# Performance work log

Hardware: AMD Instinct MI355X
Metric: run time of the kernel (lower is better)

The kernel has to match this reference:

```python
import jax, jax.numpy as jnp
import numpy as np

DIM = 1024
DIM_FEAT = 384
HIDDEN = 1024
HEADS = 16
D_HEAD = HIDDEN // HEADS
SCALE = D_HEAD ** -0.5
EPS = 1e-5


def _layernorm(x, g, b):
    mu = jnp.mean(x, axis=-1, keepdims=True)
    var = jnp.var(x, axis=-1, keepdims=True)
    return (x - mu) * jax.lax.rsqrt(var + EPS) * g + b


def _split_heads(t):
    b, n, _ = t.shape
    return t.reshape(b, n, HEADS, D_HEAD).transpose(0, 2, 1, 3)  # b h n d


def _merge_heads(t):
    b, h, n, d = t.shape
    return t.transpose(0, 2, 1, 3).reshape(b, n, h * d)


def _attn(q, k, v):
    dots = jnp.einsum('bhnd,bhmd->bhnm', q, k) * SCALE
    attn = jax.nn.softmax(dots, axis=-1)
    return jnp.einsum('bhnm,bhmd->bhnd', attn, v)


def setup_inputs() -> dict:
    key = jax.random.key(0)
    ks = jax.random.split(key, 10)
    B, N = 2, 2048
    s = lambda fan: 1.0 / np.sqrt(fan)
    return {
        'x': jax.random.normal(ks[0], (B, N, DIM), jnp.float32),
        'feature': jax.random.normal(ks[1], (B, N, DIM_FEAT), jnp.float32),
        'norm_g': jnp.ones((DIM,), jnp.float32),
        'norm_b': jnp.zeros((DIM,), jnp.float32),
        'W_cq': jax.random.normal(ks[2], (DIM, HIDDEN), jnp.float32) * s(DIM),
        'W_ckv': jax.random.normal(ks[3], (DIM_FEAT, 2 * HIDDEN), jnp.float32) * s(DIM_FEAT),
        'W_sqkv': jax.random.normal(ks[4], (DIM, 3 * HIDDEN), jnp.float32) * s(DIM),
        'ffn_g': jnp.ones((DIM,), jnp.float32),
        'ffn_b': jnp.zeros((DIM,), jnp.float32),
        'W1': jax.random.normal(ks[5], (DIM, 4 * DIM), jnp.float32) * s(DIM),
        'b1': jnp.zeros((4 * DIM,), jnp.float32),
        'W2': jax.random.normal(ks[6], (4 * DIM, DIM), jnp.float32) * s(4 * DIM),
        'b2': jnp.zeros((DIM,), jnp.float32),
    }


def reference(x, feature, norm_g, norm_b, W_cq, W_ckv, W_sqkv, ffn_g, ffn_b, W1, b1, W2, b2):
    # cross attention
    xn = _layernorm(x, norm_g, norm_b)
    q = _split_heads(xn @ W_cq)
    kv = feature @ W_ckv
    k, v = jnp.split(kv, 2, axis=-1)
    cross = _merge_heads(_attn(q, _split_heads(k), _split_heads(v))) + x
    # self attention (shared norm)
    cn = _layernorm(cross, norm_g, norm_b)
    qkv = cn @ W_sqkv
    sq, sk, sv = (_split_heads(t) for t in jnp.split(qkv, 3, axis=-1))
    self_tok = _merge_heads(_attn(sq, sk, sv)) + cross
    # FFN with its own layernorm
    h = _layernorm(self_tok, ffn_g, ffn_b)
    h = jax.nn.gelu(h @ W1 + b1, approximate=False)
    out = h @ W2 + b2
    return out + self_tok
```

## Files before the change

kernel.cpp:

```cpp
#include <hip/hip_runtime.h>
#include <math.h>
#include <stdint.h>

typedef __attribute__((ext_vector_type(8)))  short   short8;
typedef __attribute__((ext_vector_type(4)))  short   short4v;
typedef __attribute__((ext_vector_type(8)))  __bf16  bf16x8;
typedef __attribute__((ext_vector_type(4)))  float   f32x4;
typedef __attribute__((ext_vector_type(16))) float   f32x16;

__device__ __forceinline__ unsigned short f2b(float f) {
    union { float f; unsigned u; } v; v.f = f;
    unsigned r = v.u + 0x7FFF + ((v.u >> 16) & 1);
    return (unsigned short)(r >> 16);
}

__device__ __forceinline__ float b2f(unsigned short u) {
    union { unsigned u; float f; } v; v.u = (unsigned)u << 16; return v.f;
}

__device__ __forceinline__ f32x4 mfma_bf16(bf16x8 a, bf16x8 b, f32x4 c) {
    return __builtin_amdgcn_mfma_f32_16x16x32_bf16(a, b, c, 0, 0, 0);
}

__device__ __forceinline__ f32x16 mfma32(bf16x8 a, bf16x8 b, f32x16 c) {
    return __builtin_amdgcn_mfma_f32_32x32x16_bf16(a, b, c, 0, 0, 0);
}

__device__ __forceinline__ unsigned cvt_pk_bf16(float lo, float hi) {
    unsigned r;
    asm volatile("v_cvt_pk_bf16_f32 %0, %1, %2" : "=v"(r) : "v"(lo), "v"(hi));
    return r;
}

__device__ __forceinline__ void gload_lds16(const unsigned short* g, unsigned short* l) {
    __builtin_amdgcn_global_load_lds(
        (const __attribute__((address_space(1))) void*)g,
        (__attribute__((address_space(3))) void*)l,
        16, 0, 0);
}

template <int N>
__device__ __forceinline__ void wait_vmcnt() {
    if constexpr (N == 0)       asm volatile("s_waitcnt vmcnt(0)" ::: "memory");
    else if constexpr (N == 4)  asm volatile("s_waitcnt vmcnt(4)" ::: "memory");
    else if constexpr (N == 6)  asm volatile("s_waitcnt vmcnt(6)" ::: "memory");
    else if constexpr (N == 8)  asm volatile("s_waitcnt vmcnt(8)" ::: "memory");
    else                        static_assert(N == 0 || N == 4 || N == 6 || N == 8, "add vmcnt case");
}

#define QSCALE 0.18033688011112042592f

__global__ __launch_bounds__(256) void wconv_t(const float* __restrict__ W,
                                               unsigned short* __restrict__ Wt,
                                               int K, int N) {
    __shared__ float tile[32][33];
    int bk = blockIdx.x * 32;
    int bn = blockIdx.y * 32;
    int tx = threadIdx.x & 31, ty = threadIdx.x >> 5;
#pragma unroll
    for (int i = 0; i < 4; ++i) {
        int r = ty + i * 8;
        tile[r][tx] = W[(size_t)(bk + r) * N + bn + tx];
    }
    __syncthreads();
#pragma unroll
    for (int i = 0; i < 4; ++i) {
        int r = ty + i * 8;
        Wt[(size_t)(bn + r) * K + bk + tx] = f2b(tile[tx][r]);
    }
}

__global__ __launch_bounds__(256) void fconv(const float* __restrict__ in,
                                             unsigned short* __restrict__ out, int n4) {
    int i = blockIdx.x * 256 + threadIdx.x;
    if (i >= n4) return;
    f32x4 v = ((const f32x4*)in)[i];
    short4v o;
    o.x = (short)f2b(v.x); o.y = (short)f2b(v.y);
    o.z = (short)f2b(v.z); o.w = (short)f2b(v.w);
    ((short4v*)out)[i] = o;
}

__global__ __launch_bounds__(256) void lnorm(const float* __restrict__ x,
                                             const float* __restrict__ g,
                                             const float* __restrict__ bta,
                                             unsigned short* __restrict__ out) {
    int row = blockIdx.x;
    const f32x4* xr = (const f32x4*)(x + (size_t)row * 1024);
    int t = threadIdx.x;
    f32x4 v = xr[t];
    float s  = v.x + v.y + v.z + v.w;
    float s2 = v.x * v.x + v.y * v.y + v.z * v.z + v.w * v.w;
#pragma unroll
    for (int m = 1; m < 64; m <<= 1) {
        s  += __shfl_xor(s, m);
        s2 += __shfl_xor(s2, m);
    }
    __shared__ float rs[8];
    int w = t >> 6;
    if ((t & 63) == 0) { rs[w] = s; rs[4 + w] = s2; }
    __syncthreads();
    s  = rs[0] + rs[1] + rs[2] + rs[3];
    s2 = rs[4] + rs[5] + rs[6] + rs[7];
    float mean = s * (1.0f / 1024.0f);
    float var  = s2 * (1.0f / 1024.0f) - mean * mean;
    float rstd = rsqrtf(var + 1e-5f);
    f32x4 gv = ((const f32x4*)g)[t];
    f32x4 bv = ((const f32x4*)bta)[t];
    short4v o;
    o.x = (short)f2b((v.x - mean) * rstd * gv.x + bv.x);
    o.y = (short)f2b((v.y - mean) * rstd * gv.y + bv.y);
    o.z = (short)f2b((v.z - mean) * rstd * gv.z + bv.z);
    o.w = (short)f2b((v.w - mean) * rstd * gv.w + bv.w);
    ((short4v*)(out + (size_t)row * 1024))[t] = o;
}

template <int WM, int WN, int MI, int NI, int EPI, bool SCQ>
__global__ __launch_bounds__(WM * WN * 64, 2)
void gemm8(const unsigned short* __restrict__ A,
           const unsigned short* __restrict__ Bt,
           void* __restrict__ C,
           const float* __restrict__ bias,
           const float* __restrict__ resid,
           int M, int N, int K, int scale_cols) {
    constexpr int BM = WM * MI * 16;
    constexpr int BN = WN * NI * 16;
    constexpr int THREADS = WM * WN * 64;
    constexpr int ROWS = THREADS / 8;
    constexpr int IA = BM / ROWS;
    constexpr int IB = BN / ROWS;

    const int nwg = gridDim.x;
    const int nby = N / BN;
    int flat = blockIdx.x;
    int wk = (flat & 7) * (nwg >> 3) + (flat >> 3);
    const int m0 = (wk / nby) * BM;
    const int n0 = (wk % nby) * BN;

    __shared__ unsigned short As[2][BM * 64];
    __shared__ unsigned short Bs[2][BN * 64];

    const int tid  = threadIdx.x;
    const int lane = tid & 63;
    const int wid  = tid >> 6;
    const int wm = wid / WN, wn = wid % WN;
    const int l15 = lane & 15, q4 = lane >> 4, xw = lane & 7;

    const int sr = tid >> 3;
    const int sg = (tid & 7) ^ (sr & 7);

    const unsigned short* ag = A  + (size_t)(m0 + sr) * K + sg * 8;
    const unsigned short* bg = Bt + (size_t)(n0 + sr) * K + sg * 8;

    f32x4 acc[MI][NI] = {};

    auto STAGE = [&](int d, int t) {
        const int k0 = t * 64;
#pragma unroll
        for (int i = 0; i < IA; ++i)
            gload_lds16(ag + (size_t)(i * ROWS) * K + k0, &As[d][i * ROWS * 64 + tid * 8]);
#pragma unroll
        for (int i = 0; i < IB; ++i)
            gload_lds16(bg + (size_t)(i * ROWS) * K + k0, &Bs[d][i * ROWS * 64 + tid * 8]);
    };

    const int NT = K >> 6;
    STAGE(0, 0);

    for (int t = 0; t < NT; ++t) {
        const int c = t & 1;
        if (t + 1 < NT) STAGE(c ^ 1, t + 1);
        __builtin_amdgcn_sched_barrier(0);
        if (t + 1 < NT) wait_vmcnt<IA + IB>();
        else            wait_vmcnt<0>();
        __builtin_amdgcn_s_barrier();
        __builtin_amdgcn_sched_barrier(0);
#pragma unroll
        for (int h = 0; h < 2; ++h) {
            bf16x8 a[MI], b[NI];
            const int gsl = h * 4 + q4;
#pragma unroll
            for (int mi = 0; mi < MI; ++mi)
                a[mi] = *(const bf16x8*)&As[c][(wm * MI * 16 + mi * 16 + l15) * 64 + ((gsl ^ xw) << 3)];
#pragma unroll
            for (int ni = 0; ni < NI; ++ni)
                b[ni] = *(const bf16x8*)&Bs[c][(wn * NI * 16 + ni * 16 + l15) * 64 + ((gsl ^ xw) << 3)];
            __builtin_amdgcn_s_setprio(1);
#pragma unroll
            for (int mi = 0; mi < MI; ++mi)
#pragma unroll
                for (int ni = 0; ni < NI; ++ni)
                    acc[mi][ni] = mfma_bf16(a[mi], b[ni], acc[mi][ni]);
            __builtin_amdgcn_s_setprio(0);
        }
        __builtin_amdgcn_sched_barrier(0);
        __builtin_amdgcn_s_barrier();
    }

    const int rb = m0 + wm * MI * 16 + q4 * 4;
    const int cb = n0 + wn * NI * 16 + l15;
    float bv[NI];
    if (EPI >= 1) {
#pragma unroll
        for (int ni = 0; ni < NI; ++ni) bv[ni] = bias[cb + ni * 16];
    }
#pragma unroll
    for (int mi = 0; mi < MI; ++mi) {
#pragma unroll
        for (int r = 0; r < 4; ++r) {
            const int row = rb + mi * 16 + r;
#pragma unroll
            for (int ni = 0; ni < NI; ++ni) {
                const int col = cb + ni * 16;
                float v = acc[mi][ni][r];
                if (EPI == 0) {
                    if (SCQ && col < scale_cols) v *= QSCALE;
                    ((unsigned short*)C)[(size_t)row * N + col] = f2b(v);
                } else if (EPI == 1) {
                    v += bv[ni];
                    v = 0.5f * v * (1.0f + erff(v * 0.70710678118f));
                    ((unsigned short*)C)[(size_t)row * N + col] = f2b(v);
                } else {
                    v += bv[ni] + resid[(size_t)row * N + col];
                    ((float*)C)[(size_t)row * N + col] = v;
                }
            }
        }
    }
}

template <int EPI, bool SCQ, int KSPLIT>
__global__ __launch_bounds__(512, 2)
void gemm256(const unsigned short* __restrict__ A,
             const unsigned short* __restrict__ Bt,
             void* __restrict__ C,
             const float* __restrict__ bias,
             unsigned short* __restrict__ ph0,
             unsigned short* __restrict__ ph1,
             int M, int N, int lda, int ldb, int klen, int scale_cols) {
    const int nby = N / 256;
    const int nmn = (M / 256) * nby;
    const int nwg = gridDim.x;
    int flat = blockIdx.x;
    int wk = (flat & 7) * (nwg >> 3) + (flat >> 3);
    int ks = 0;
    if constexpr (KSPLIT > 1) { ks = wk / nmn; wk -= ks * nmn; }
    const int m0 = (wk / nby) * 256;
    const int n0 = (wk % nby) * 256;
    const int koff = ks * klen;

    __shared__ unsigned short As[2][256 * 64];
    __shared__ unsigned short Bs[2][256 * 64];

    const int tid  = threadIdx.x;
    const int lane = tid & 63;
    const int wid  = tid >> 6;
    const int wm = wid >> 2, wn = wid & 3;
    const int l15 = lane & 15, q4 = lane >> 4, xw = lane & 7;

    const int sr = tid >> 3;
    const int sg = (tid & 7) ^ (sr & 7);

    const unsigned short* ag = A  + (size_t)(m0 + sr) * lda + koff + sg * 8;
    const unsigned short* bg = Bt + (size_t)(n0 + sr) * ldb + koff + sg * 8;

    f32x4 acc[8][4] = {};

#define SA256(d, t, i) gload_lds16(ag + (size_t)((i) * 64) * lda + (t) * 64, &As[d][(i) * 4096 + tid * 8])
#define SB256(d, t, i) gload_lds16(bg + (size_t)((i) * 64) * ldb + (t) * 64, &Bs[d][(i) * 4096 + tid * 8])

    const int NT = klen >> 6;
#pragma unroll
    for (int i = 0; i < 4; ++i) { SA256(0, 0, i); SB256(0, 0, i); }
    __syncthreads();

    for (int t = 0; t < NT; ++t) {
        const int c = t & 1;
        if (t + 1 < NT) {
#pragma unroll
            for (int i = 0; i < 4; ++i) { SA256(c ^ 1, t + 1, i); SB256(c ^ 1, t + 1, i); }
        }
        bf16x8 breg[4];
#pragma unroll
        for (int p = 0; p < 4; ++p) {
            const int h = p >> 1, mh = p & 1;
            const int col = ((h * 4 + q4) ^ xw) << 3;
            if ((p & 1) == 0) {
#pragma unroll
                for (int ni = 0; ni < 4; ++ni)
                    breg[ni] = *(const bf16x8*)&Bs[c][(wn * 64 + ni * 16 + l15) * 64 + col];
            }
            bf16x8 a[4];
#pragma unroll
            for (int mi = 0; mi < 4; ++mi)
                a[mi] = *(const bf16x8*)&As[c][(wm * 128 + mh * 64 + mi * 16 + l15) * 64 + col];
#pragma unroll
            for (int mi = 0; mi < 4; ++mi)
#pragma unroll
                for (int ni = 0; ni < 4; ++ni)
                    acc[mh * 4 + mi][ni] = mfma_bf16(a[mi], breg[ni], acc[mh * 4 + mi][ni]);
        }
        __syncthreads();
    }
#undef SA256
#undef SB256

    const int rb = m0 + wm * 128 + q4 * 4;
    const int cb = n0 + wn * 64 + l15;
    float bv[4];
    if (EPI == 1) {
#pragma unroll
        for (int ni = 0; ni < 4; ++ni) bv[ni] = bias[cb + ni * 16];
    }
    unsigned short* pb = nullptr;
    if (EPI == 3) pb = ((ks & 2) ? ph1 : ph0) + (size_t)(ks & 1) * ((size_t)M * N);
#pragma unroll
    for (int ai = 0; ai < 8; ++ai) {
#pragma unroll
        for (int r = 0; r < 4; ++r) {
            const int row = rb + ai * 16 + r;
#pragma unroll
            for (int ni = 0; ni < 4; ++ni) {
                const int col = cb + ni * 16;
                float v = acc[ai][ni][r];
                if (EPI == 0) {
                    if (SCQ && col < scale_cols) v *= QSCALE;
                    ((unsigned short*)C)[(size_t)row * N + col] = f2b(v);
                } else if (EPI == 1) {
                    v += bv[ni];
                    v = 0.5f * v * (1.0f + erff(v * 0.70710678118f));
                    ((unsigned short*)C)[(size_t)row * N + col] = f2b(v);
                } else {
                    pb[(size_t)row * N + col] = f2b(v);
                }
            }
        }
    }
}

__global__ __launch_bounds__(256) void kmerge(const unsigned short* __restrict__ p01,
                                              const unsigned short* __restrict__ p23,
                                              const float* __restrict__ bias,
                                              float* __restrict__ out) {
    const size_t i4 = (size_t)blockIdx.x * 256 + threadIdx.x;
    const size_t e = i4 * 4;
    const int col4 = (int)(e & 1023);
    f32x4 acc = *(const f32x4*)&bias[col4];
    const size_t MN = (size_t)4096 * 1024;
#pragma unroll
    for (int k = 0; k < 2; ++k) {
        short4v a = *(const short4v*)&p01[k * MN + e];
        short4v b = *(const short4v*)&p23[k * MN + e];
        acc.x += b2f((unsigned short)a.x) + b2f((unsigned short)b.x);
        acc.y += b2f((unsigned short)a.y) + b2f((unsigned short)b.y);
        acc.z += b2f((unsigned short)a.z) + b2f((unsigned short)b.z);
        acc.w += b2f((unsigned short)a.w) + b2f((unsigned short)b.w);
    }
    f32x4 o = *(const f32x4*)&out[e];
    o.x += acc.x; o.y += acc.y; o.z += acc.z; o.w += acc.w;
    *(f32x4*)&out[e] = o;
}

__global__ __launch_bounds__(256) void kvpack(const unsigned short* __restrict__ src,
                                              int stride, int k_off, int v_off,
                                              unsigned short* __restrict__ pack) {
    const int oct = blockIdx.x;
    const int bh  = blockIdx.y;
    const int b = bh >> 4, h = bh & 15;
    const int tid = threadIdx.x;
    const int lane = tid & 63;
    const int sl = tid >> 6;
    const int l31 = lane & 31, l5 = lane >> 5;
    __shared__ unsigned short Kl[32 * 64], Vl[32 * 64];
    const int r = tid >> 3, c8 = (tid & 7) * 8;
    for (int t8 = 0; t8 < 8; ++t8) {
        const int kt = oct * 8 + t8;
        const int kb = kt * 32;
        *(short8*)&Kl[r * 64 + c8] = *(const short8*)&src[(size_t)(b * 2048 + kb + r) * stride + k_off + h * 64 + c8];
        *(short8*)&Vl[r * 64 + c8] = *(const short8*)&src[(size_t)(b * 2048 + kb + r) * stride + v_off + h * 64 + c8];
        __syncthreads();
        unsigned short* o = pack + (size_t)bh * 262144 + (size_t)kt * 4096;
        *(short8*)&o[sl * 512 + lane * 8] = *(const short8*)&Kl[l31 * 64 + sl * 16 + l5 * 8];
        {
            const int dh = sl >> 1, c2 = sl & 1;
            short8 vv;
#pragma unroll
            for (int j = 0; j < 8; ++j)
                vv[j] = (short)Vl[(c2 * 16 + l5 * 8 + j) * 64 + dh * 32 + l31];
            *(short8*)&o[(4 + sl) * 512 + lane * 8] = vv;
        }
        __syncthreads();
    }
}

__global__ __launch_bounds__(256) void attn(const unsigned short* __restrict__ Q, int q_stride, int q_off,
                                            const unsigned short* __restrict__ pack,
                                            const float* __restrict__ res,
                                            float* __restrict__ out) {
    const int bid = blockIdx.x;
    const int slot = bid >> 3;
    const int bh = (bid & 7) * 4 + (slot >> 5);
    const int qt = slot & 31;
    const int b = bh >> 4, h = bh & 15;
    const int tid = threadIdx.x;
    const int lane = tid & 63, w = tid >> 6;
    const int qg = w >> 1, ks = w & 1;
    const int l31 = lane & 31, l5 = lane >> 5;

    __shared__ unsigned short lds[2][8192];

    const int q0 = qt * 64 + qg * 32;

    const unsigned short* qp = Q + (size_t)(b * 2048 + q0 + l31) * q_stride + q_off + h * 64 + l5 * 8;
    bf16x8 qf[4];
#pragma unroll
    for (int i = 0; i < 4; ++i) qf[i] = *(const bf16x8*)&qp[i * 16];

    const unsigned short* pkb = pack + (size_t)bh * 262144;

    f32x16 oacc[2] = {};
    f32x16 lacc = {};

    auto STAGE = [&](int d, int t) {
        const unsigned short* s = pkb + (size_t)t * 8192;
#pragma unroll
        for (int i = 0; i < 4; ++i) {
            const int ch = i * 4 + w;
            gload_lds16(s + ch * 512 + lane * 8, &lds[d][ch * 512 + lane * 8]);
        }
    };

    STAGE(0, 0);

    for (int t = 0; t < 32; ++t) {
        const int cur = t & 1;
        if (t + 1 < 32) STAGE(cur ^ 1, t + 1);
        __builtin_amdgcn_sched_barrier(0);
        if (t + 1 < 32) wait_vmcnt<4>();
        else            wait_vmcnt<0>();
        __builtin_amdgcn_s_barrier();
        __builtin_amdgcn_sched_barrier(0);

        const unsigned short* L = &lds[cur][ks * 4096 + lane * 8];

        bf16x8 kf[4];
#pragma unroll
        for (int i = 0; i < 4; ++i) kf[i] = *(const bf16x8*)&L[i * 512];

        f32x16 s = {};
        __builtin_amdgcn_s_setprio(1);
#pragma unroll
        for (int i = 0; i < 4; ++i) s = mfma32(kf[i], qf[i], s);
        __builtin_amdgcn_s_setprio(0);

        bf16x8 vf[2][2];
#pragma unroll
        for (int dh = 0; dh < 2; ++dh)
#pragma unroll
            for (int c2 = 0; c2 < 2; ++c2)
                vf[dh][c2] = *(const bf16x8*)&L[(4 + dh * 2 + c2) * 512];

        float p[16];
#pragma unroll
        for (int r = 0; r < 16; ++r) p[r] = __builtin_amdgcn_exp2f(s[r]);
#pragma unroll
        for (int r = 0; r < 16; ++r) lacc[r] += p[r];

        bf16x8 pf[2];
#pragma unroll
        for (int c = 0; c < 2; ++c) {
            unsigned a0 = cvt_pk_bf16(p[8 * c + 0], p[8 * c + 1]);
            unsigned a1 = cvt_pk_bf16(p[8 * c + 4], p[8 * c + 5]);
            unsigned b0 = cvt_pk_bf16(p[8 * c + 2], p[8 * c + 3]);
            unsigned b1 = cvt_pk_bf16(p[8 * c + 6], p[8 * c + 7]);
            asm volatile("v_permlane32_swap_b32 %0, %1" : "+v"(a0), "+v"(a1));
            asm volatile("v_permlane32_swap_b32 %0, %1" : "+v"(b0), "+v"(b1));
            union { unsigned u[4]; bf16x8 v; } pu;
            pu.u[0] = a0; pu.u[1] = b0; pu.u[2] = a1; pu.u[3] = b1;
            pf[c] = pu.v;
        }

        __builtin_amdgcn_s_setprio(1);
#pragma unroll
        for (int dh = 0; dh < 2; ++dh)
#pragma unroll
            for (int c2 = 0; c2 < 2; ++c2)
                oacc[dh] = mfma32(vf[dh][c2], pf[c2], oacc[dh]);
        __builtin_amdgcn_s_setprio(0);

        __builtin_amdgcn_s_barrier();
    }

    float lsum[16];
#pragma unroll
    for (int r = 0; r < 16; ++r) lsum[r] = lacc[r];
#pragma unroll
    for (int off = 8; off >= 1; off >>= 1)
#pragma unroll
        for (int r = 0; r < off; ++r) lsum[r] += lsum[r + off];
    float lh = lsum[0] + __shfl_xor(lsum[0], 32);

    float* mb = (float*)&lds[qg][0];
    if (ks == 1) {
#pragma unroll
        for (int dh = 0; dh < 2; ++dh)
#pragma unroll
            for (int r = 0; r < 16; ++r)
                mb[lane * 33 + dh * 16 + r] = oacc[dh][r];
        mb[lane * 33 + 32] = lh;
    }
    __syncthreads();
    if (ks == 0) {
#pragma unroll
        for (int dh = 0; dh < 2; ++dh)
#pragma unroll
            for (int r = 0; r < 16; ++r)
                oacc[dh][r] += mb[lane * 33 + dh * 16 + r];
        const float l = lh + mb[lane * 33 + 32];

        const float inv = 1.0f / l;
        const size_t rowoff = (size_t)(b * 2048 + q0 + l31) * 1024 + h * 64;
#pragma unroll
        for (int dh = 0; dh < 2; ++dh) {
#pragma unroll
            for (int g = 0; g < 4; ++g) {
                const int col = dh * 32 + g * 8 + l5 * 4;
                f32x4 rv = *(const f32x4*)&res[rowoff + col];
                f32x4 ov;
#pragma unroll
                for (int r = 0; r < 4; ++r) ov[r] = oacc[dh][g * 4 + r] * inv + rv[r];
                *(f32x4*)&out[rowoff + col] = ov;
            }
        }
    }
}

extern "C" void kernel_launch(void* const* d_in, const int* in_sizes, int n_in,
                              void* d_out, int out_size, void* d_ws, size_t ws_size,
                              hipStream_t stream) {
    const float* x      = (const float*)d_in[0];
    const float* feat   = (const float*)d_in[1];
    const float* norm_g = (const float*)d_in[2];
    const float* norm_b = (const float*)d_in[3];
    const float* W_cq   = (const float*)d_in[4];
    const float* W_ckv  = (const float*)d_in[5];
    const float* W_sqkv = (const float*)d_in[6];
    const float* ffn_g  = (const float*)d_in[7];
    const float* ffn_b  = (const float*)d_in[8];
    const float* W1     = (const float*)d_in[9];
    const float* b1     = (const float*)d_in[10];
    const float* W2     = (const float*)d_in[11];
    const float* b2     = (const float*)d_in[12];
    float* out = (float*)d_out;

    char* ws = (char*)d_ws;
    unsigned short* wq_t   = (unsigned short*)(ws + (size_t)(0u)   * (1u << 20));
    unsigned short* wkv_t  = (unsigned short*)(ws + (size_t)(2u)   * (1u << 20));
    unsigned short* wqkv_t = (unsigned short*)(ws + (size_t)(4u)   * (1u << 20));
    unsigned short* w1_t   = (unsigned short*)(ws + (size_t)(10u)  * (1u << 20));
    unsigned short* w2_t   = (unsigned short*)(ws + (size_t)(18u)  * (1u << 20));
    unsigned short* featb  = (unsigned short*)(ws + (size_t)(26u)  * (1u << 20));
    unsigned short* t0     = (unsigned short*)(ws + (size_t)(29u)  * (1u << 20));
    float*          cross  = (float*)        (ws + (size_t)(37u)  * (1u << 20));
    unsigned short* qb     = (unsigned short*)(ws + (size_t)(53u)  * (1u << 20));
    unsigned short* kvb    = (unsigned short*)(ws + (size_t)(61u)  * (1u << 20));
    unsigned short* qkvb   = (unsigned short*)(ws + (size_t)(77u)  * (1u << 20));
    unsigned short* packb  = (unsigned short*)(ws + (size_t)(101u) * (1u << 20));
    unsigned short* h1     = (unsigned short*)(ws + (size_t)(53u)  * (1u << 20));
    unsigned short* part01 = (unsigned short*)(ws + (size_t)(37u)  * (1u << 20));
    unsigned short* part23 = (unsigned short*)(ws + (size_t)(101u) * (1u << 20));

    wconv_t<<<dim3(1024 / 32, 1024 / 32), 256, 0, stream>>>(W_cq,   wq_t,   1024, 1024);
    wconv_t<<<dim3(384 / 32,  2048 / 32), 256, 0, stream>>>(W_ckv,  wkv_t,  384,  2048);
    wconv_t<<<dim3(1024 / 32, 3072 / 32), 256, 0, stream>>>(W_sqkv, wqkv_t, 1024, 3072);
    wconv_t<<<dim3(1024 / 32, 4096 / 32), 256, 0, stream>>>(W1,     w1_t,   1024, 4096);
    wconv_t<<<dim3(4096 / 32, 1024 / 32), 256, 0, stream>>>(W2,     w2_t,   4096, 1024);
    fconv<<<dim3((4096 * 384 / 4) / 256), 256, 0, stream>>>(feat, featb, 4096 * 384 / 4);

    lnorm<<<4096, 256, 0, stream>>>(x, norm_g, norm_b, t0);
    gemm8<2, 2, 4, 2, 0, true ><<<512, 256, 0, stream>>>(t0,    wq_t,  qb,  nullptr, nullptr, 4096, 1024, 1024, 1024);
    gemm8<2, 2, 4, 4, 0, false><<<512, 256, 0, stream>>>(featb, wkv_t, kvb, nullptr, nullptr, 4096, 2048, 384,  0);
    kvpack<<<dim3(8, 32), 256, 0, stream>>>(kvb, 2048, 0, 1024, packb);
    attn<<<1024, 256, 0, stream>>>(qb, 1024, 0, packb, x, cross);

    lnorm<<<4096, 256, 0, stream>>>(cross, norm_g, norm_b, t0);
    gemm256<0, true , 1><<<192, 512, 0, stream>>>(t0, wqkv_t, qkvb, nullptr, nullptr, nullptr, 4096, 3072, 1024, 1024, 1024, 1024);
    kvpack<<<dim3(8, 32), 256, 0, stream>>>(qkvb, 3072, 1024, 2048, packb);
    attn<<<1024, 256, 0, stream>>>(qkvb, 3072, 0, packb, cross, out);

    lnorm<<<4096, 256, 0, stream>>>(out, ffn_g, ffn_b, t0);
    gemm256<1, false, 1><<<256, 512, 0, stream>>>(t0, w1_t, h1, b1, nullptr, nullptr, 4096, 4096, 1024, 1024, 1024, 0);
    gemm256<3, false, 4><<<256, 512, 0, stream>>>(h1, w2_t, nullptr, nullptr, part01, part23, 4096, 1024, 4096, 4096, 1024, 0);
    kmerge<<<4096, 256, 0, stream>>>(part01, part23, b2, out);
}
```

Baseline: 329.7 us.

## Split 256x256 GEMM tiles into half-buffers with phased prefetch and vmcnt waits

Restructures the 256x256 bf16 GEMM main loop into four phases. Each phase loads one 128-row half of A or B for the next k-step, waits with a fine-grained vmcnt instead of a full __syncthreads, and raises wave priority around its MFMA block. The warp-to-output mapping also changes, so each wave now owns four 16-row blocks in each M half and two 16-column blocks in each N half. The aim is to overlap global-to-LDS loads with MFMA work and cut barrier stalls, at the cost of more barriers per k-step and a more fragile wait-count scheme.

New measurement: 322.6 us, median of 4. -2.2%, faster.

```diff
diff --git a/kernel.cpp b/kernel.cpp
--- a/kernel.cpp
+++ b/kernel.cpp
@@ -42,10 +42,11 @@
 template <int N>
 __device__ __forceinline__ void wait_vmcnt() {
     if constexpr (N == 0)       asm volatile("s_waitcnt vmcnt(0)" ::: "memory");
+    else if constexpr (N == 2)  asm volatile("s_waitcnt vmcnt(2)" ::: "memory");
     else if constexpr (N == 4)  asm volatile("s_waitcnt vmcnt(4)" ::: "memory");
     else if constexpr (N == 6)  asm volatile("s_waitcnt vmcnt(6)" ::: "memory");
     else if constexpr (N == 8)  asm volatile("s_waitcnt vmcnt(8)" ::: "memory");
-    else                        static_assert(N == 0 || N == 4 || N == 6 || N == 8, "add vmcnt case");
+    else                        static_assert(N <= 8, "add vmcnt case");
 }
 
 #define QSCALE 0.18033688011112042592f
@@ -249,8 +250,8 @@
     const int n0 = (wk % nby) * 256;
     const int koff = ks * klen;
 
-    __shared__ unsigned short As[2][256 * 64];
-    __shared__ unsigned short Bs[2][256 * 64];
+    __shared__ unsigned short Ah[2][2][128 * 64];
+    __shared__ unsigned short Bh[2][2][128 * 64];
 
     const int tid  = threadIdx.x;
     const int lane = tid & 63;
@@ -266,51 +267,77 @@
 
     f32x4 acc[8][4] = {};
 
-#define SA256(d, t, i) gload_lds16(ag + (size_t)((i) * 64) * lda + (t) * 64, &As[d][(i) * 4096 + tid * 8])
-#define SB256(d, t, i) gload_lds16(bg + (size_t)((i) * 64) * ldb + (t) * 64, &Bs[d][(i) * 4096 + tid * 8])
+    auto SA = [&](int d, int half, int t) {
+#pragma unroll
+        for (int i = 0; i < 2; ++i)
+            gload_lds16(ag + (size_t)(half * 128 + i * 64) * lda + t * 64,
+                        &Ah[d][half][i * 4096 + tid * 8]);
+    };
+    auto SB = [&](int d, int half, int t) {
+#pragma unroll
+        for (int i = 0; i < 2; ++i)
+            gload_lds16(bg + (size_t)(half * 128 + i * 64) * ldb + t * 64,
+                        &Bh[d][half][i * 4096 + tid * 8]);
+    };
 
     const int NT = klen >> 6;
-#pragma unroll
-    for (int i = 0; i < 4; ++i) { SA256(0, 0, i); SB256(0, 0, i); }
-    __syncthreads();
+    SA(0, 0, 0); SB(0, 0, 0); SA(0, 1, 0); SB(0, 1, 0);
+    wait_vmcnt<4>();
+    __builtin_amdgcn_s_barrier();
+
+    bf16x8 bb[2][2];
+
+#define PHASE256(P, NH, MH, TAILW)                                                      \
+    {                                                                                   \
+        if (MH == 0) {                                                                  \
+            _Pragma("unroll") for (int ni = 0; ni < 2; ++ni)                            \
+            _Pragma("unroll") for (int kx = 0; kx < 2; ++kx)                            \
+                bb[ni][kx] = *(const bf16x8*)&Bh[c][NH][                                \
+                    (wn * 32 + ni * 16 + l15) * 64 + (((kx * 4 + q4) ^ xw) << 3)];      \
+        }                                                                               \
+        bf16x8 aa[4][2];                                                                \
+        _Pragma("unroll") for (int mi = 0; mi < 4; ++mi)                                \
+        _Pragma("unroll") for (int kx = 0; kx < 2; ++kx)                                \
+            aa[mi][kx] = *(const bf16x8*)&Ah[c][MH][                                    \
+                (wm * 64 + mi * 16 + l15) * 64 + (((kx * 4 + q4) ^ xw) << 3)];          \
+        if (pf) {                                                                       \
+            if (P == 0)      SA(c ^ 1, 0, t + 1);                                       \
+            else if (P == 1) SB(c ^ 1, 0, t + 1);                                       \
+            else if (P == 2) SA(c ^ 1, 1, t + 1);                                       \
+            else             SB(c ^ 1, 1, t + 1);                                       \
+        }                                                                               \
+        __builtin_amdgcn_sched_barrier(0);                                              \
+        if (pf) wait_vmcnt<4>(); else wait_vmcnt<TAILW>();                              \
+        __builtin_amdgcn_s_barrier();                                                   \
+        asm volatile("s_waitcnt lgkmcnt(0)" ::: "memory");                              \
+        __builtin_amdgcn_sched_barrier(0);                                              \
+        __builtin_amdgcn_s_setprio(1);                                                  \
+        _Pragma("unroll") for (int mi = 0; mi < 4; ++mi)                                \
+        _Pragma("unroll") for (int ni = 0; ni < 2; ++ni)                                \
+        _Pragma("unroll") for (int kx = 0; kx < 2; ++kx)                                \
+            acc[MH * 4 + mi][NH * 2 + ni] =                                             \
+                mfma_bf16(aa[mi][kx], bb[ni][kx], acc[MH * 4 + mi][NH * 2 + ni]);       \
+        __builtin_amdgcn_s_setprio(0);                                                  \
+        __builtin_amdgcn_sched_barrier(0);                                              \
+    }
 
     for (int t = 0; t < NT; ++t) {
         const int c = t & 1;
-        if (t + 1 < NT) {
-#pragma unroll
-            for (int i = 0; i < 4; ++i) { SA256(c ^ 1, t + 1, i); SB256(c ^ 1, t + 1, i); }
-        }
-        bf16x8 breg[4];
-#pragma unroll
-        for (int p = 0; p < 4; ++p) {
-            const int h = p >> 1, mh = p & 1;
-            const int col = ((h * 4 + q4) ^ xw) << 3;
-            if ((p & 1) == 0) {
-#pragma unroll
-                for (int ni = 0; ni < 4; ++ni)
-                    breg[ni] = *(const bf16x8*)&Bs[c][(wn * 64 + ni * 16 + l15) * 64 + col];
-            }
-            bf16x8 a[4];
-#pragma unroll
-            for (int mi = 0; mi < 4; ++mi)
-                a[mi] = *(const bf16x8*)&As[c][(wm * 128 + mh * 64 + mi * 16 + l15) * 64 + col];
-#pragma unroll
-            for (int mi = 0; mi < 4; ++mi)
-#pragma unroll
-                for (int ni = 0; ni < 4; ++ni)
-                    acc[mh * 4 + mi][ni] = mfma_bf16(a[mi], breg[ni], acc[mh * 4 + mi][ni]);
-        }
-        __syncthreads();
-    }
-#undef SA256
-#undef SB256
-
-    const int rb = m0 + wm * 128 + q4 * 4;
-    const int cb = n0 + wn * 64 + l15;
+        const bool pf = (t + 1 < NT);
+        PHASE256(0, 0, 0, 2)
+        PHASE256(1, 0, 1, 0)
+        PHASE256(2, 1, 0, 0)
+        PHASE256(3, 1, 1, 0)
+    }
+#undef PHASE256
+
+    const int rbb = m0 + wm * 64 + q4 * 4;
+    const int cbb = n0 + wn * 32 + l15;
     float bv[4];
     if (EPI == 1) {
 #pragma unroll
-        for (int ni = 0; ni < 4; ++ni) bv[ni] = bias[cb + ni * 16];
+        for (int bi = 0; bi < 4; ++bi)
+            bv[bi] = bias[cbb + (bi >> 1) * 128 + (bi & 1) * 16];
     }
     unsigned short* pb = nullptr;
     if (EPI == 3) pb = ((ks & 2) ? ph1 : ph0) + (size_t)(ks & 1) * ((size_t)M * N);
@@ -318,16 +345,16 @@
     for (int ai = 0; ai < 8; ++ai) {
 #pragma unroll
         for (int r = 0; r < 4; ++r) {
-            const int row = rb + ai * 16 + r;
-#pragma unroll
-            for (int ni = 0; ni < 4; ++ni) {
-                const int col = cb + ni * 16;
-                float v = acc[ai][ni][r];
+            const int row = rbb + (ai >> 2) * 128 + (ai & 3) * 16 + r;
+#pragma unroll
+            for (int bi = 0; bi < 4; ++bi) {
+                const int col = cbb + (bi >> 1) * 128 + (bi & 1) * 16;
+                float v = acc[ai][bi][r];
                 if (EPI == 0) {
                     if (SCQ && col < scale_cols) v *= QSCALE;
                     ((unsigned short*)C)[(size_t)row * N + col] = f2b(v);
                 } else if (EPI == 1) {
-                    v += bv[ni];
+                    v += bv[bi];
                     v = 0.5f * v * (1.0f + erff(v * 0.70710678118f));
                     ((unsigned short*)C)[(size_t)row * N + col] = f2b(v);
                 } else {
```
